# Performance work log

Hardware: AMD Instinct MI355X
Metric: run time of the kernel (lower is better)

The kernel has to match this reference:

```python
import jax, jax.numpy as jnp
import numpy as np

EPS = 1e-5


def bn_relu(h, gamma, beta):
    # BatchNorm1d in training mode (batch stats over node dim) + ReLU
    mu = jnp.mean(h, axis=0)
    var = jnp.var(h, axis=0)
    return jax.nn.relu(gamma * (h - mu) * jax.lax.rsqrt(var + EPS) + beta)


def rel_graph_conv(x, src, dst, etypes, W, loopW, bias, num_nodes):
    # transform-then-gather: cheaper than per-edge matmul since N < E
    h_all = jnp.einsum('ni,rio->rno', x, W)          # [R, N, out]
    msg = h_all[etypes, src]                          # [E, out] gather
    agg = jax.ops.segment_sum(msg, dst, num_segments=num_nodes)  # scatter-sum
    return agg + x @ loopW + bias


def setup_inputs() -> dict:
    key = jax.random.key(0)
    ks = jax.random.split(key, 10)
    N, E, R, F_in, H, L = 100000, 1600000, 4, 64, 128, 2
    s = 1.0 / np.sqrt(H)
    return {
        'x': jax.random.normal(ks[0], (N, F_in), jnp.float32),
        'src': jax.random.randint(ks[1], (E,), 0, N, jnp.int32),
        'dst': jax.random.randint(ks[2], (E,), 0, N, jnp.int32),
        'etypes': jax.random.randint(ks[3], (E,), 0, R, jnp.int32),
        'W0': jax.random.normal(ks[4], (R, F_in, H), jnp.float32) / np.sqrt(F_in),
        'loop0': jax.random.normal(ks[5], (F_in, H), jnp.float32) / np.sqrt(F_in),
        'b0': jnp.zeros((H,), jnp.float32),
        'g0': jnp.ones((H,), jnp.float32),
        'be0': jnp.zeros((H,), jnp.float32),
        'Ws': jax.random.normal(ks[6], (L, R, H, H), jnp.float32) * s,
        'loops': jax.random.normal(ks[7], (L, H, H), jnp.float32) * s,
        'bs': jnp.zeros((L, H), jnp.float32),
        'gs': jnp.ones((L, H), jnp.float32),
        'bes': jnp.zeros((L, H), jnp.float32),
        'Wl': jax.random.normal(ks[8], (H, H), jnp.float32) * s,
        'bl': jnp.zeros((H,), jnp.float32),
        'gl': jnp.ones((H,), jnp.float32),
        'bel': jnp.zeros((H,), jnp.float32),
    }


def reference(x, src, dst, etypes, W0, loop0, b0, g0, be0,
              Ws, loops, bs, gs, bes, Wl, bl, gl, bel):
    N = x.shape[0]
    h = bn_relu(rel_graph_conv(x, src, dst, etypes, W0, loop0, b0, N), g0, be0)
    for l in range(Ws.shape[0]):  # small fixed number of layers
        h = bn_relu(rel_graph_conv(h, src, dst, etypes, Ws[l], loops[l], bs[l], N), gs[l], bes[l])
    # last_layer: Linear + BatchNorm (no ReLU)
    h = h @ Wl + bl
    mu = jnp.mean(h, axis=0)
    var = jnp.var(h, axis=0)
    return gl * (h - mu) * jax.lax.rsqrt(var + EPS) + bel
```

## Files before the change

### kernel.cpp

```cpp
#include <hip/hip_runtime.h>

constexpr int H = 128;
constexpr int EPB = 8192;
constexpr int BSH = 8;
constexpr int NSHADOW = 32;

typedef __attribute__((ext_vector_type(8))) __bf16 bf16x8;
typedef __attribute__((ext_vector_type(4))) float  f32x4;

__device__ __forceinline__ unsigned short f2bf(float f) {
  unsigned u = __builtin_bit_cast(unsigned, f);
  u += 0x7FFFu + ((u >> 16) & 1u);
  return (unsigned short)(u >> 16);
}
__device__ __forceinline__ float bf2f(unsigned short b) {
  unsigned u = ((unsigned)b) << 16;
  return __builtin_bit_cast(float, u);
}
__device__ __forceinline__ unsigned pk2(float2 a) {
  return (unsigned)f2bf(a.x) | ((unsigned)f2bf(a.y) << 16);
}

__global__ void zero_k(float* p, int n) {
  const int i = blockIdx.x * 256 + threadIdx.x;
  if (i < n) p[i] = 0.f;
}

__global__ __launch_bounds__(256) void prep_wcat_k(
    const float* __restrict__ Wr, const float* __restrict__ loopW,
    unsigned short* __restrict__ Bpre, int K, int segShift, int nRel)
{
  const int idx = blockIdx.x * 256 + threadIdx.x;
  const int S = K / 32;
  const int total = 8 * S * 64;
  if (idx >= total) return;
  const int lane = idx & 63;
  const int s    = (idx >> 6) % S;
  const int Ct   = idx / (S * 64);
  const int col  = Ct * 16 + (lane & 15);
  const int k0   = s * 32 + (lane >> 4) * 8;
  const int seg  = k0 >> segShift;
  const int segK = 1 << segShift;
  const int kk   = k0 & (segK - 1);
  const float* src = (seg < nRel) ? (Wr + ((size_t)seg * segK + kk) * H + col)
                                  : (loopW + (size_t)kk * H + col);
  unsigned short v[8];
#pragma unroll
  for (int j = 0; j < 8; ++j) v[j] = f2bf(src[(size_t)j * H]);
  unsigned short* dst = Bpre + (size_t)((Ct * S + s) * 64 + lane) * 8;
  *(uint4*)dst = *(uint4*)v;
}

__global__ __launch_bounds__(256) void bucket_hist_k(
    const int* __restrict__ dst, int E, int* __restrict__ gcnt, int nbuckets)
{
  __shared__ int cnt[512];
  const int tid = threadIdx.x;
  for (int b = tid; b < nbuckets; b += 256) cnt[b] = 0;
  __syncthreads();
  const int base = blockIdx.x * EPB;
  for (int j = tid; j < EPB; j += 256) {
    const int e = base + j;
    if (e < E) atomicAdd(&cnt[dst[e] >> BSH], 1);
  }
  __syncthreads();
  for (int b = tid; b < nbuckets; b += 256)
    if (cnt[b]) atomicAdd(&gcnt[b], cnt[b]);
}

__global__ __launch_bounds__(512) void bucket_scan_k(
    const int* __restrict__ gcnt, int* __restrict__ boffs,
    int* __restrict__ pcur, int nbuckets, int E)
{
  __shared__ int s[512];
  const int t = threadIdx.x;
  const int x = (t < nbuckets) ? gcnt[t] : 0;
  s[t] = x; __syncthreads();
  for (int off = 1; off < 512; off <<= 1) {
    const int v = (t >= off) ? s[t - off] : 0;
    __syncthreads(); s[t] += v; __syncthreads();
  }
  if (t < nbuckets) {
    const int excl = s[t] - x;
    boffs[t] = excl;
    pcur[t * 16] = excl;
  }
  if (t == 0) boffs[nbuckets] = E;
}

__global__ __launch_bounds__(256) void pack2_k(
    const int* __restrict__ src, const int* __restrict__ dst,
    const int* __restrict__ et, int E,
    int* __restrict__ pcur, int* __restrict__ ep_log, int nbuckets)
{
  __shared__ int cnt[512];
  __shared__ int basel[512];
  __shared__ unsigned short ranks[EPB];
  const int tid = threadIdx.x;
  for (int b = tid; b < nbuckets; b += 256) cnt[b] = 0;
  __syncthreads();
  const int base = blockIdx.x * EPB;
  for (int j = tid; j < EPB; j += 256) {
    const int e = base + j;
    if (e < E) ranks[j] = (unsigned short)atomicAdd(&cnt[dst[e] >> BSH], 1);
  }
  __syncthreads();
  for (int b = tid; b < nbuckets; b += 256)
    basel[b] = cnt[b] ? atomicAdd(&pcur[b * 16], cnt[b]) : 0;
  __syncthreads();
  for (int j = tid; j < EPB; j += 256) {
    const int e = base + j;
    if (e < E) {
      const int d = dst[e];
      const int pos = basel[d >> BSH] + ranks[j];
      ep_log[pos] = ((d & 255) << 19) | (et[e] << 17) | src[e];
    }
  }
}

__global__ __launch_bounds__(256) void bucket_sort2_k(
    const int* __restrict__ boffs, const int* __restrict__ ep_log,
    int* __restrict__ ep, int* __restrict__ rowp, int Nn, int E)
{
  __shared__ int ent[EPB];
  __shared__ int cntA[256];
  __shared__ int curA[256];
  const int b = blockIdx.x;
  const int tid = threadIdx.x;
  const int beg = boffs[b], end = boffs[b + 1];
  const int n = end - beg;
  const bool inl = (n <= EPB);
  if (inl) for (int i = tid; i < n; i += 256) ent[i] = ep_log[beg + i];
  cntA[tid] = 0;
  __syncthreads();
  for (int i = tid; i < n; i += 256) {
    const int v = inl ? ent[i] : ep_log[beg + i];
    atomicAdd(&cntA[v >> 19], 1);
  }
  __syncthreads();
  const int my = cntA[tid];
  for (int off = 1; off < 256; off <<= 1) {
    const int v = (tid >= off) ? cntA[tid - off] : 0;
    __syncthreads(); cntA[tid] += v; __syncthreads();
  }
  const int excl = cntA[tid] - my;
  const int node = (b << BSH) + tid;
  if (node < Nn) rowp[node] = beg + excl;
  if (b == 0 && tid == 0) rowp[Nn] = E;
  curA[tid] = excl;
  __syncthreads();
  for (int i = tid; i < n; i += 256) {
    const int v = inl ? ent[i] : ep_log[beg + i];
    const int p = atomicAdd(&curA[v >> 19], 1);
    ep[beg + p] = v & 0x7FFFF;
  }
}

__global__ __launch_bounds__(256) void cvt_x_k(
    const float* __restrict__ x, unsigned short* __restrict__ xb, int nchunks)
{
  const int i = blockIdx.x * 256 + threadIdx.x;
  if (i >= nchunks) return;
  const float4 v = ((const float4*)x)[i];
  unsigned short o[4] = { f2bf(v.x), f2bf(v.y), f2bf(v.z), f2bf(v.w) };
  *(uint2*)(xb + (size_t)i * 4) = *(uint2*)o;
}

template<int DCOLS>
__global__ __launch_bounds__(256) void gather4_k(
    const unsigned short* __restrict__ hsrc,
    const int* __restrict__ rowp, const int* __restrict__ ep,
    unsigned short* __restrict__ aggcat,
    int Nn)
{
  const int tid = threadIdx.x;
  const int wave = tid >> 6, lane = tid & 63;
  const int waveId = blockIdx.x * 4 + wave;
  const int nWaves = gridDim.x * 4;
  for (int node = waveId; node < Nn; node += nWaves) {
    const int beg = rowp[node], end = rowp[node + 1];
    float2 a0{0.f,0.f}, a1{0.f,0.f}, a2{0.f,0.f}, a3{0.f,0.f};
    int e = beg, cnt = end - beg;
    while (cnt > 0) {
      const int take = cnt < 64 ? cnt : 64;
      const int pv = (lane < take) ? ep[e + lane] : 0;
      for (int j0 = 0; j0 < take; j0 += 8) {
        const int m = take - j0;
        if (m >= 8) {
          int pj[8];
#pragma unroll
          for (int j = 0; j < 8; ++j) pj[j] = __shfl(pv, j0 + j);
          if constexpr (DCOLS == 128) {
            unsigned vv[8];
#pragma unroll
            for (int j = 0; j < 8; ++j)
              vv[j] = *(const unsigned*)(hsrc + (size_t)(pj[j] & 0x1FFFF) * DCOLS + lane * 2);
#pragma unroll
            for (int j = 0; j < 8; ++j) {
              const float vx = bf2f((unsigned short)(vv[j] & 0xFFFF));
              const float vy = bf2f((unsigned short)(vv[j] >> 16));
              switch (pj[j] >> 17) {
                case 0:  a0.x += vx; a0.y += vy; break;
                case 1:  a1.x += vx; a1.y += vy; break;
                case 2:  a2.x += vx; a2.y += vy; break;
                default: a3.x += vx; a3.y += vy; break;
              }
            }
          } else {
            unsigned short vv[8];
#pragma unroll
            for (int j = 0; j < 8; ++j)
              vv[j] = hsrc[(size_t)(pj[j] & 0x1FFFF) * DCOLS + lane];
#pragma unroll
            for (int j = 0; j < 8; ++j) {
              const float vx = bf2f(vv[j]);
              switch (pj[j] >> 17) {
                case 0:  a0.x += vx; break;
                case 1:  a1.x += vx; break;
                case 2:  a2.x += vx; break;
                default: a3.x += vx; break;
              }
            }
          }
        } else {
          for (int j = 0; j < m; ++j) {
            const int p = __shfl(pv, j0 + j);
            const int r = p >> 17;
            const int s = p & 0x1FFFF;
            if constexpr (DCOLS == 128) {
              const unsigned v = *(const unsigned*)(hsrc + (size_t)s * DCOLS + lane * 2);
              const float vx = bf2f((unsigned short)(v & 0xFFFF));
              const float vy = bf2f((unsigned short)(v >> 16));
              switch (r) {
                case 0:  a0.x += vx; a0.y += vy; break;
                case 1:  a1.x += vx; a1.y += vy; break;
                case 2:  a2.x += vx; a2.y += vy; break;
                default: a3.x += vx; a3.y += vy; break;
              }
            } else {
              const float vx = bf2f(hsrc[(size_t)s * DCOLS + lane]);
              switch (r) {
                case 0:  a0.x += vx; break;
                case 1:  a1.x += vx; break;
                case 2:  a2.x += vx; break;
                default: a3.x += vx; break;
              }
            }
          }
        }
      }
      e += take; cnt -= take;
    }
    if constexpr (DCOLS == 128) {
      unsigned* orow = (unsigned*)(aggcat + (size_t)node * 512);
      orow[lane]       = pk2(a0);
      orow[64  + lane] = pk2(a1);
      orow[128 + lane] = pk2(a2);
      orow[192 + lane] = pk2(a3);
    } else {
      unsigned short* orow = aggcat + (size_t)node * 256;
      orow[lane]       = f2bf(a0.x);
      orow[64  + lane] = f2bf(a1.x);
      orow[128 + lane] = f2bf(a2.x);
      orow[192 + lane] = f2bf(a3.x);
    }
  }
}

template<int KTILE>
__global__ __launch_bounds__(256) void mfma_cat_t(
    const unsigned short* __restrict__ A0, const unsigned short* __restrict__ A1,
    const unsigned short* __restrict__ Bpre, const float* __restrict__ bias,
    float* __restrict__ shadow, float* __restrict__ pre,
    int M, int W0, int D1, int nkt)
{
  constexpr int KS = KTILE / 32;
  constexpr int strideL = KTILE + 8;
  constexpr int CPR = KTILE / 8;
  constexpr int NR  = (128 * CPR) / 256;
  __shared__ unsigned short Alds[2][128 * strideL];
  __shared__ float sred[128], qred[128];
  const int tid = threadIdx.x;
  const int wave = tid >> 6, lane = tid & 63;
  const int quad = lane >> 4, l15 = lane & 15;
  const int rowBase = blockIdx.x * 128;
  const int S = nkt * KS;
  if (tid < 128) { sred[tid] = 0.f; qred[tid] = 0.f; }

  uint4 R[NR];

  auto stage_load = [&](int kt) {
    const int kbase = kt * KTILE;
    const unsigned short* base; int stride, koff;
    if (kbase < W0) { base = A0; stride = W0; koff = kbase; }
    else            { base = A1; stride = D1; koff = kbase - W0; }
#pragma unroll
    for (int i = 0; i < NR; ++i) {
      const int c = tid + i * 256;
      const int row = c / CPR, ch = c % CPR;
      const int grow = rowBase + row;
      R[i] = make_uint4(0u, 0u, 0u, 0u);
      if (grow < M)
        R[i] = *(const uint4*)(base + (size_t)grow * stride + koff + ch * 8);
    }
  };
  auto stage_write = [&](int buf) {
#pragma unroll
    for (int i = 0; i < NR; ++i) {
      const int c = tid + i * 256;
      const int row = c / CPR, ch = c % CPR;
      *(uint4*)(&Alds[buf][row * strideL + ch * 8]) = R[i];
    }
  };

  stage_load(0);
  stage_write(0);
  __syncthreads();

  f32x4 acc[2][8] = {};
  int cur = 0;
  for (int kt = 0; kt < nkt; ++kt) {
    if (kt + 1 < nkt) stage_load(kt + 1);
#pragma unroll
    for (int s = 0; s < KS; ++s) {
      const bf16x8 a0f = *(const bf16x8*)(&Alds[cur][(wave * 32 + l15) * strideL + s * 32 + quad * 8]);
      const bf16x8 a1f = *(const bf16x8*)(&Alds[cur][(wave * 32 + 16 + l15) * strideL + s * 32 + quad * 8]);
      const int sg = kt * KS + s;
#pragma unroll
      for (int ct = 0; ct < 8; ++ct) {
        const bf16x8 b = *(const bf16x8*)(Bpre + (size_t)((ct * S + sg) * 64 + lane) * 8);
        acc[0][ct] = __builtin_amdgcn_mfma_f32_16x16x32_bf16(a0f, b, acc[0][ct], 0, 0, 0);
        acc[1][ct] = __builtin_amdgcn_mfma_f32_16x16x32_bf16(a1f, b, acc[1][ct], 0, 0, 0);
      }
    }
    if (kt + 1 < nkt) stage_write(cur ^ 1);
    __syncthreads();
    cur ^= 1;
  }

  float bia[8];
#pragma unroll
  for (int ct = 0; ct < 8; ++ct) bia[ct] = bias[ct * 16 + l15];
  float s8[8], q8[8];
#pragma unroll
  for (int ct = 0; ct < 8; ++ct) { s8[ct] = 0.f; q8[ct] = 0.f; }
#pragma unroll
  for (int rt = 0; rt < 2; ++rt) {
#pragma unroll
    for (int reg = 0; reg < 4; ++reg) {
      const int row = rowBase + wave * 32 + rt * 16 + quad * 4 + reg;
      if (row < M) {
#pragma unroll
        for (int ct = 0; ct < 8; ++ct) {
          const float v = acc[rt][ct][reg] + bia[ct];
          pre[(size_t)row * H + ct * 16 + l15] = v;
          s8[ct] += v; q8[ct] += v * v;
        }
      }
    }
  }
#pragma unroll
  for (int ct = 0; ct < 8; ++ct) {
    s8[ct] += __shfl_xor(s8[ct], 16); s8[ct] += __shfl_xor(s8[ct], 32);
    q8[ct] += __shfl_xor(q8[ct], 16); q8[ct] += __shfl_xor(q8[ct], 32);
  }
  if (quad == 0) {
#pragma unroll
    for (int ct = 0; ct < 8; ++ct) {
      atomicAdd(&sred[ct * 16 + l15], s8[ct]);
      atomicAdd(&qred[ct * 16 + l15], q8[ct]);
    }
  }
  __syncthreads();
  if (tid < 128) {
    float* sh = shadow + (size_t)(blockIdx.x & (NSHADOW - 1)) * 256;
    atomicAdd(&sh[tid], sred[tid]);
    atomicAdd(&sh[128 + tid], qred[tid]);
  }
}

__global__ void bn_coef_k(const float* __restrict__ shadow,
                          const float* __restrict__ gamma, const float* __restrict__ beta,
                          float* __restrict__ st, float invN)
{
  const int t = threadIdx.x;
  float su = 0.f, qu = 0.f;
  for (int c = 0; c < NSHADOW; ++c) { su += shadow[c * 256 + t]; qu += shadow[c * 256 + 128 + t]; }
  const float mu  = su * invN;
  const float var = qu * invN - mu * mu;
  const float s = gamma[t] * rsqrtf(var + 1e-5f);
  st[t] = s; st[128 + t] = beta[t] - s * mu;
}

template<int RELU>
__global__ __launch_bounds__(256) void bn_apply_t(
    const float* __restrict__ pre, const float* __restrict__ st,
    unsigned short* __restrict__ hout, float* __restrict__ fout, int nchunks)
{
  __shared__ float ss[128], tt[128];
  if (threadIdx.x < 128) { ss[threadIdx.x] = st[threadIdx.x]; tt[threadIdx.x] = st[128 + threadIdx.x]; }
  __syncthreads();
  const int i = blockIdx.x * 256 + threadIdx.x;
  if (i >= nchunks) return;
  const float4 v = ((const float4*)pre)[i];
  const int col0 = (i & 31) * 4;
  float y0 = fmaf(ss[col0 + 0], v.x, tt[col0 + 0]);
  float y1 = fmaf(ss[col0 + 1], v.y, tt[col0 + 1]);
  float y2 = fmaf(ss[col0 + 2], v.z, tt[col0 + 2]);
  float y3 = fmaf(ss[col0 + 3], v.w, tt[col0 + 3]);
  if (RELU) {
    unsigned short o[4] = { f2bf(fmaxf(y0, 0.f)), f2bf(fmaxf(y1, 0.f)),
                            f2bf(fmaxf(y2, 0.f)), f2bf(fmaxf(y3, 0.f)) };
    *(uint2*)(hout + (size_t)i * 4) = *(uint2*)o;
  } else {
    ((float4*)fout)[i] = make_float4(y0, y1, y2, y3);
  }
}

extern "C" void kernel_launch(void* const* d_in, const int* in_sizes, int n_in,
                              void* d_out, int out_size, void* d_ws, size_t ws_size,
                              hipStream_t stream)
{
  const float* x     = (const float*)d_in[0];
  const int*   src   = (const int*)d_in[1];
  const int*   dst   = (const int*)d_in[2];
  const int*   et    = (const int*)d_in[3];
  const float* W0    = (const float*)d_in[4];
  const float* loop0 = (const float*)d_in[5];
  const float* b0    = (const float*)d_in[6];
  const float* g0    = (const float*)d_in[7];
  const float* be0   = (const float*)d_in[8];
  const float* Ws    = (const float*)d_in[9];
  const float* loops = (const float*)d_in[10];
  const float* bs    = (const float*)d_in[11];
  const float* gs    = (const float*)d_in[12];
  const float* bes   = (const float*)d_in[13];
  const float* Wl    = (const float*)d_in[14];
  const float* bl    = (const float*)d_in[15];
  const float* gl    = (const float*)d_in[16];
  const float* bel   = (const float*)d_in[17];

  const int E = in_sizes[1];
  const int F_in = 64;
  const int N = in_sizes[0] / F_in;
  const int R = in_sizes[4] / (F_in * H);
  const int L = in_sizes[9] / (R * H * H);
  const float invN = 1.0f / (float)N;

  float* outp = (float*)d_out;

  char* p = (char*)d_ws;
  auto alloc = [&](size_t bytes) { char* r = p; p += (bytes + 255) & ~size_t(255); return r; };
  const int nbuckets = (N + (1 << BSH) - 1) >> BSH;
  const int shadowN = NSHADOW * 256;
  const int c0 = 8 * (320 / 32) * 64 * 8;
  const int ch = 8 * (640 / 32) * 64 * 8;
  const int cf = 8 * (128 / 32) * 64 * 8;
  float*          pre      = (float*)alloc((size_t)N * H * 4);
  float*          shadow   = (float*)alloc((size_t)(L + 2) * shadowN * 4);
  float*          st       = (float*)alloc((size_t)(L + 2) * 256 * 4);
  unsigned short* aggcat   = (unsigned short*)alloc((size_t)N * 4 * H * 2);
  unsigned short* xb       = (unsigned short*)alloc((size_t)N * F_in * 2);
  unsigned short* hbuf     = (unsigned short*)alloc((size_t)N * H * 2);
  unsigned short* Bpre_all = (unsigned short*)alloc((size_t)(c0 + L * ch + cf) * 2);
  int*            gcnt     = (int*)alloc((size_t)nbuckets * 4);
  int*            boffs    = (int*)alloc((size_t)(nbuckets + 1) * 4);
  int*            pcur     = (int*)alloc((size_t)nbuckets * 16 * 4);
  int*            rowp     = (int*)alloc((size_t)(N + 1) * 4);
  int*            ep       = (int*)alloc((size_t)E * 4);
  int*            ep_log   = (int*)pre;
  (void)ws_size;

  const int pblocks = (E + EPB - 1) / EPB;
  const int rowBlocks = (N + 127) / 128;

  hipLaunchKernelGGL(prep_wcat_k, dim3((8 * 10 * 64 + 255) / 256), dim3(256), 0, stream,
                     W0, loop0, Bpre_all, 320, 6, R);
  for (int l = 0; l < L; ++l)
    hipLaunchKernelGGL(prep_wcat_k, dim3((8 * 20 * 64 + 255) / 256), dim3(256), 0, stream,
                       Ws + (size_t)l * R * H * H, loops + (size_t)l * H * H,
                       Bpre_all + (size_t)(c0 + l * ch), 640, 7, R);
  hipLaunchKernelGGL(prep_wcat_k, dim3((8 * 4 * 64 + 255) / 256), dim3(256), 0, stream,
                     (const float*)nullptr, Wl, Bpre_all + (size_t)(c0 + L * ch), 128, 7, 0);

  {
    const int nz = (L + 2) * shadowN;
    hipLaunchKernelGGL(zero_k, dim3((nz + 255) / 256), dim3(256), 0, stream, shadow, nz);
  }
  hipLaunchKernelGGL(zero_k, dim3((nbuckets + 255) / 256), dim3(256), 0, stream,
                     (float*)gcnt, nbuckets);

  hipLaunchKernelGGL(bucket_hist_k, dim3(pblocks), dim3(256), 0, stream, dst, E, gcnt, nbuckets);
  hipLaunchKernelGGL(bucket_scan_k, dim3(1), dim3(512), 0, stream, gcnt, boffs, pcur, nbuckets, E);
  hipLaunchKernelGGL(pack2_k, dim3(pblocks), dim3(256), 0, stream,
                     src, dst, et, E, pcur, ep_log, nbuckets);
  hipLaunchKernelGGL(bucket_sort2_k, dim3(nbuckets), dim3(256), 0, stream,
                     boffs, ep_log, ep, rowp, N, E);

  hipLaunchKernelGGL(cvt_x_k, dim3((N * 16 + 255) / 256), dim3(256), 0, stream,
                     x, xb, N * 16);

  const int applyBlocks = (N * 32 + 255) / 256;

  hipLaunchKernelGGL((gather4_k<64>), dim3(2048), dim3(256), 0, stream,
                     xb, rowp, ep, aggcat, N);
  hipLaunchKernelGGL((mfma_cat_t<64>), dim3(rowBlocks), dim3(256), 0, stream,
                     aggcat, xb, Bpre_all, b0, shadow, pre, N, 4 * F_in, F_in, 5);
  hipLaunchKernelGGL(bn_coef_k, dim3(1), dim3(128), 0, stream, shadow, g0, be0, st, invN);
  hipLaunchKernelGGL((bn_apply_t<1>), dim3(applyBlocks), dim3(256), 0, stream,
                     pre, st, hbuf, (float*)nullptr, N * 32);

  for (int l = 0; l < L; ++l) {
    hipLaunchKernelGGL((gather4_k<128>), dim3(2048), dim3(256), 0, stream,
                       hbuf, rowp, ep, aggcat, N);
    hipLaunchKernelGGL((mfma_cat_t<128>), dim3(rowBlocks), dim3(256), 0, stream,
                       aggcat, hbuf, Bpre_all + (size_t)(c0 + l * ch), bs + (size_t)l * H,
                       shadow + (size_t)(1 + l) * shadowN, pre, N, 4 * H, H, 5);
    hipLaunchKernelGGL(bn_coef_k, dim3(1), dim3(128), 0, stream,
                       shadow + (size_t)(1 + l) * shadowN, gs + (size_t)l * H, bes + (size_t)l * H,
                       st + (size_t)(1 + l) * 256, invN);
    hipLaunchKernelGGL((bn_apply_t<1>), dim3(applyBlocks), dim3(256), 0, stream,
                       pre, st + (size_t)(1 + l) * 256, hbuf, (float*)nullptr, N * 32);
  }

  hipLaunchKernelGGL((mfma_cat_t<128>), dim3(rowBlocks), dim3(256), 0, stream,
                     (const unsigned short*)nullptr, hbuf, Bpre_all + (size_t)(c0 + L * ch), bl,
                     shadow + (size_t)(1 + L) * shadowN, pre, N, 0, H, 1);
  hipLaunchKernelGGL(bn_coef_k, dim3(1), dim3(128), 0, stream,
                     shadow + (size_t)(1 + L) * shadowN, gl, bel,
                     st + (size_t)(1 + L) * 256, invN);
  hipLaunchKernelGGL((bn_apply_t<0>), dim3(applyBlocks), dim3(256), 0, stream,
                     pre, st + (size_t)(1 + L) * 256, (unsigned short*)nullptr, outp, N * 32);
}
```

Measured before the change: 799.5 us.

## Sort edges by (dst, relation) so gather drops per-edge relation switch

The in-bucket sort now keys on node and relation type together (1024 sub-buckets per block), producing a CSR with four row pointers per node, one per relation. The gather kernel loops over each relation's segment and accumulates into a single register pair, removing the per-edge switch on relation and the masking of the source index. This cuts divergent branching and register pressure in the gather at the cost of a four-times larger row-pointer array, four separate loops per node with more tail iterations, and a slightly heavier scan in the sort kernel.

Result: no change. 784.8 us (-1.8%).

```diff
diff --git a/kernel.cpp b/kernel.cpp
--- a/kernel.cpp
+++ b/kernel.cpp
@@ -120,39 +120,53 @@
 
 __global__ __launch_bounds__(256) void bucket_sort2_k(
     const int* __restrict__ boffs, const int* __restrict__ ep_log,
-    int* __restrict__ ep, int* __restrict__ rowp, int Nn, int E)
+    int* __restrict__ ep, int* __restrict__ rowp4, int Nn, int E)
 {
   __shared__ int ent[EPB];
-  __shared__ int cntA[256];
-  __shared__ int curA[256];
+  __shared__ int cntA[1024];
+  __shared__ int curA[1024];
+  __shared__ int tsum[256];
   const int b = blockIdx.x;
   const int tid = threadIdx.x;
   const int beg = boffs[b], end = boffs[b + 1];
   const int n = end - beg;
   const bool inl = (n <= EPB);
   if (inl) for (int i = tid; i < n; i += 256) ent[i] = ep_log[beg + i];
-  cntA[tid] = 0;
+  for (int k = tid; k < 1024; k += 256) cntA[k] = 0;
   __syncthreads();
   for (int i = tid; i < n; i += 256) {
     const int v = inl ? ent[i] : ep_log[beg + i];
-    atomicAdd(&cntA[v >> 19], 1);
-  }
-  __syncthreads();
-  const int my = cntA[tid];
+    atomicAdd(&cntA[v >> 17], 1);
+  }
+  __syncthreads();
+  const int c0 = cntA[tid * 4], c1 = cntA[tid * 4 + 1];
+  const int c2 = cntA[tid * 4 + 2], c3 = cntA[tid * 4 + 3];
+  const int s1 = c0 + c1, s2 = s1 + c2;
+  const int T = s2 + c3;
+  tsum[tid] = T;
+  __syncthreads();
   for (int off = 1; off < 256; off <<= 1) {
-    const int v = (tid >= off) ? cntA[tid - off] : 0;
-    __syncthreads(); cntA[tid] += v; __syncthreads();
-  }
-  const int excl = cntA[tid] - my;
+    const int v = (tid >= off) ? tsum[tid - off] : 0;
+    __syncthreads(); tsum[tid] += v; __syncthreads();
+  }
+  const int eb = tsum[tid] - T;
+  curA[tid * 4]     = eb;
+  curA[tid * 4 + 1] = eb + c0;
+  curA[tid * 4 + 2] = eb + s1;
+  curA[tid * 4 + 3] = eb + s2;
   const int node = (b << BSH) + tid;
-  if (node < Nn) rowp[node] = beg + excl;
-  if (b == 0 && tid == 0) rowp[Nn] = E;
-  curA[tid] = excl;
+  if (node < Nn) {
+    rowp4[node * 4]     = beg + eb;
+    rowp4[node * 4 + 1] = beg + eb + c0;
+    rowp4[node * 4 + 2] = beg + eb + s1;
+    rowp4[node * 4 + 3] = beg + eb + s2;
+  }
+  if (b == 0 && tid == 0) rowp4[(size_t)Nn * 4] = E;
   __syncthreads();
   for (int i = tid; i < n; i += 256) {
     const int v = inl ? ent[i] : ep_log[beg + i];
-    const int p = atomicAdd(&curA[v >> 19], 1);
-    ep[beg + p] = v & 0x7FFFF;
+    const int p = atomicAdd(&curA[v >> 17], 1);
+    ep[beg + p] = v & 0x1FFFF;
   }
 }
 
@@ -169,7 +183,7 @@
 template<int DCOLS>
 __global__ __launch_bounds__(256) void gather4_k(
     const unsigned short* __restrict__ hsrc,
-    const int* __restrict__ rowp, const int* __restrict__ ep,
+    const int* __restrict__ rowp4, const int* __restrict__ ep,
     unsigned short* __restrict__ aggcat,
     int Nn)
 {
@@ -178,15 +192,20 @@
   const int waveId = blockIdx.x * 4 + wave;
   const int nWaves = gridDim.x * 4;
   for (int node = waveId; node < Nn; node += nWaves) {
-    const int beg = rowp[node], end = rowp[node + 1];
-    float2 a0{0.f,0.f}, a1{0.f,0.f}, a2{0.f,0.f}, a3{0.f,0.f};
-    int e = beg, cnt = end - beg;
-    while (cnt > 0) {
-      const int take = cnt < 64 ? cnt : 64;
-      const int pv = (lane < take) ? ep[e + lane] : 0;
-      for (int j0 = 0; j0 < take; j0 += 8) {
-        const int m = take - j0;
-        if (m >= 8) {
+    int rs[5];
+#pragma unroll
+    for (int i = 0; i < 5; ++i) rs[i] = rowp4[node * 4 + i];
+    float2 av[4];
+#pragma unroll
+    for (int r = 0; r < 4; ++r) {
+      int e = rs[r];
+      const int rend = rs[r + 1];
+      float2 a{0.f, 0.f};
+      while (e < rend) {
+        const int take = (rend - e) < 64 ? (rend - e) : 64;
+        const int pv = (lane < take) ? ep[e + lane] : 0;
+        int j0 = 0;
+        for (; j0 + 8 <= take; j0 += 8) {
           int pj[8];
 #pragma unroll
           for (int j = 0; j < 8; ++j) pj[j] = __shfl(pv, j0 + j);
@@ -194,75 +213,43 @@
             unsigned vv[8];
 #pragma unroll
             for (int j = 0; j < 8; ++j)
-              vv[j] = *(const unsigned*)(hsrc + (size_t)(pj[j] & 0x1FFFF) * DCOLS + lane * 2);
+              vv[j] = *(const unsigned*)(hsrc + (size_t)pj[j] * DCOLS + lane * 2);
 #pragma unroll
             for (int j = 0; j < 8; ++j) {
-              const float vx = bf2f((unsigned short)(vv[j] & 0xFFFF));
-              const float vy = bf2f((unsigned short)(vv[j] >> 16));
-              switch (pj[j] >> 17) {
-                case 0:  a0.x += vx; a0.y += vy; break;
-                case 1:  a1.x += vx; a1.y += vy; break;
-                case 2:  a2.x += vx; a2.y += vy; break;
-                default: a3.x += vx; a3.y += vy; break;
-              }
+              a.x += bf2f((unsigned short)(vv[j] & 0xFFFF));
+              a.y += bf2f((unsigned short)(vv[j] >> 16));
             }
           } else {
             unsigned short vv[8];
 #pragma unroll
             for (int j = 0; j < 8; ++j)
-              vv[j] = hsrc[(size_t)(pj[j] & 0x1FFFF) * DCOLS + lane];
-#pragma unroll
-            for (int j = 0; j < 8; ++j) {
-              const float vx = bf2f(vv[j]);
-              switch (pj[j] >> 17) {
-                case 0:  a0.x += vx; break;
-                case 1:  a1.x += vx; break;
-                case 2:  a2.x += vx; break;
-                default: a3.x += vx; break;
-              }
-            }
-          }
-        } else {
-          for (int j = 0; j < m; ++j) {
-            const int p = __shfl(pv, j0 + j);
-            const int r = p >> 17;
-            const int s = p & 0x1FFFF;
-            if constexpr (DCOLS == 128) {
-              const unsigned v = *(const unsigned*)(hsrc + (size_t)s * DCOLS + lane * 2);
-              const float vx = bf2f((unsigned short)(v & 0xFFFF));
-              const float vy = bf2f((unsigned short)(v >> 16));
-              switch (r) {
-                case 0:  a0.x += vx; a0.y += vy; break;
-                case 1:  a1.x += vx; a1.y += vy; break;
-                case 2:  a2.x += vx; a2.y += vy; break;
-                default: a3.x += vx; a3.y += vy; break;
-              }
-            } else {
-              const float vx = bf2f(hsrc[(size_t)s * DCOLS + lane]);
-              switch (r) {
-                case 0:  a0.x += vx; break;
-                case 1:  a1.x += vx; break;
-                case 2:  a2.x += vx; break;
-                default: a3.x += vx; break;
-              }
-            }
+              vv[j] = hsrc[(size_t)pj[j] * DCOLS + lane];
+#pragma unroll
+            for (int j = 0; j < 8; ++j) a.x += bf2f(vv[j]);
           }
         }
+        for (; j0 < take; ++j0) {
+          const int s = __shfl(pv, j0);
+          if constexpr (DCOLS == 128) {
+            const unsigned v = *(const unsigned*)(hsrc + (size_t)s * DCOLS + lane * 2);
+            a.x += bf2f((unsigned short)(v & 0xFFFF));
+            a.y += bf2f((unsigned short)(v >> 16));
+          } else {
+            a.x += bf2f(hsrc[(size_t)s * DCOLS + lane]);
+          }
+        }
+        e += take;
       }
-      e += take; cnt -= take;
+      av[r] = a;
     }
     if constexpr (DCOLS == 128) {
       unsigned* orow = (unsigned*)(aggcat + (size_t)node * 512);
-      orow[lane]       = pk2(a0);
-      orow[64  + lane] = pk2(a1);
-      orow[128 + lane] = pk2(a2);
-      orow[192 + lane] = pk2(a3);
+#pragma unroll
+      for (int r = 0; r < 4; ++r) orow[r * 64 + lane] = pk2(av[r]);
     } else {
       unsigned short* orow = aggcat + (size_t)node * 256;
-      orow[lane]       = f2bf(a0.x);
-      orow[64  + lane] = f2bf(a1.x);
-      orow[128 + lane] = f2bf(a2.x);
-      orow[192 + lane] = f2bf(a3.x);
+#pragma unroll
+      for (int r = 0; r < 4; ++r) orow[r * 64 + lane] = f2bf(av[r].x);
     }
   }
 }
@@ -466,7 +453,7 @@
   int*            gcnt     = (int*)alloc((size_t)nbuckets * 4);
   int*            boffs    = (int*)alloc((size_t)(nbuckets + 1) * 4);
   int*            pcur     = (int*)alloc((size_t)nbuckets * 16 * 4);
-  int*            rowp     = (int*)alloc((size_t)(N + 1) * 4);
+  int*            rowp4    = (int*)alloc(((size_t)N * 4 + 1) * 4);
   int*            ep       = (int*)alloc((size_t)E * 4);
   int*            ep_log   = (int*)pre;
   (void)ws_size;
@@ -495,7 +482,7 @@
   hipLaunchKernelGGL(pack2_k, dim3(pblocks), dim3(256), 0, stream,
                      src, dst, et, E, pcur, ep_log, nbuckets);
   hipLaunchKernelGGL(bucket_sort2_k, dim3(nbuckets), dim3(256), 0, stream,
-                     boffs, ep_log, ep, rowp, N, E);
+                     boffs, ep_log, ep, rowp4, N, E);
 
   hipLaunchKernelGGL(cvt_x_k, dim3((N * 16 + 255) / 256), dim3(256), 0, stream,
                      x, xb, N * 16);
@@ -503,7 +490,7 @@
   const int applyBlocks = (N * 32 + 255) / 256;
 
   hipLaunchKernelGGL((gather4_k<64>), dim3(2048), dim3(256), 0, stream,
-                     xb, rowp, ep, aggcat, N);
+                     xb, rowp4, ep, aggcat, N);
   hipLaunchKernelGGL((mfma_cat_t<64>), dim3(rowBlocks), dim3(256), 0, stream,
                      aggcat, xb, Bpre_all, b0, shadow, pre, N, 4 * F_in, F_in, 5);
   hipLaunchKernelGGL(bn_coef_k, dim3(1), dim3(128), 0, stream, shadow, g0, be0, st, invN);
@@ -512,7 +499,7 @@
 
   for (int l = 0; l < L; ++l) {
     hipLaunchKernelGGL((gather4_k<128>), dim3(2048), dim3(256), 0, stream,
-                       hbuf, rowp, ep, aggcat, N);
+                       hbuf, rowp4, ep, aggcat, N);
     hipLaunchKernelGGL((mfma_cat_t<128>), dim3(rowBlocks), dim3(256), 0, stream,
                        aggcat, hbuf, Bpre_all + (size_t)(c0 + l * ch), bs + (size_t)l * H,
                        shadow + (size_t)(1 + l) * shadowN, pre, N, 4 * H, H, 5);
```
